# Performance work log

Measured on AMD Instinct MI355X. Metric: run time of the kernel, lower is better.

Reference implementation:

```python
import jax, jax.numpy as jnp
import numpy as np

COMMITMENT_COST = 0.25
NUM_EMBEDDINGS = 8192
EMBEDDING_DIM = 256


def setup_inputs() -> dict:
    key = jax.random.key(0)
    kx, ke = jax.random.split(key)
    x = jax.random.normal(kx, (16, 1024, EMBEDDING_DIM), dtype=jnp.float32)
    # nn.Embedding weight initialized uniform(-1/K, 1/K)
    embedding = jax.random.uniform(
        ke, (NUM_EMBEDDINGS, EMBEDDING_DIM), dtype=jnp.float32,
        minval=-1.0 / NUM_EMBEDDINGS, maxval=1.0 / NUM_EMBEDDINGS)
    return {"x": x, "embedding": embedding}


def reference(x, embedding):
    x_shape = x.shape
    D = embedding.shape[1]
    K = embedding.shape[0]
    flat_x = x.reshape(-1, D)                      # [N, D]
    N = flat_x.shape[0]

    distances = (jnp.sum(flat_x ** 2, axis=1, keepdims=True)
                 + jnp.sum(embedding ** 2, axis=1)
                 - 2.0 * jnp.matmul(flat_x, embedding.T))
    encoding_indices = jnp.argmin(distances, axis=1)  # [N]

    # one-hot @ embedding == gather
    quantized = embedding[encoding_indices].reshape(x_shape)

    sg = jax.lax.stop_gradient
    e_latent_loss = jnp.mean((sg(quantized) - x) ** 2)
    q_latent_loss = jnp.mean((quantized - sg(x)) ** 2)
    loss = q_latent_loss + COMMITMENT_COST * e_latent_loss

    # straight-through estimator
    quantized_st = x + sg(quantized - x)

    # perplexity from mean one-hot usage
    counts = jnp.zeros((K,), dtype=jnp.float32).at[encoding_indices].add(1.0)
    avg_probs = counts / N
    perplexity = jnp.exp(-jnp.sum(avg_probs * jnp.log(avg_probs + 1e-10)))

    return quantized_st.reshape(x_shape), loss, perplexity
```

## Files before the change

### kernel.cpp

```cpp
#include <hip/hip_runtime.h>


#define VQ_N 16384
#define VQ_D 256
#define VQ_K 8192

typedef __attribute__((ext_vector_type(4))) int i32x4;

#define SX 22.0f
#define SEF 1040384.0f
#define ENSCALE 11444224.0

__device__ inline int q8(float f, float scale) {
  return __float2int_rn(fminf(fmaxf(f * scale, -127.f), 127.f));
}

__global__ __launch_bounds__(256) void vq_pack(
    const float* __restrict__ E, signed char* __restrict__ Ebs,
    int* __restrict__ en_int, double* __restrict__ loss_sum,
    int* __restrict__ hist, unsigned int* __restrict__ ticket) {
  const int gid = blockIdx.x * 256 + threadIdx.x;
  if (gid < VQ_K) hist[gid] = 0;
  if (gid == 0) { *loss_sum = 0.0; *ticket = 0u; }
  const int code = gid >> 4;
  const int chunk = gid & 15;
  const float* src = E + (size_t)code * VQ_D + chunk * 16;
  double s = 0.0;
  unsigned int w[4];
#pragma unroll
  for (int v = 0; v < 4; ++v) {
    const float4 f = *(const float4*)(src + v * 4);
    s += (double)f.x * f.x + (double)f.y * f.y + (double)f.z * f.z +
         (double)f.w * f.w;
    const int q0 = q8(f.x, SEF), q1 = q8(f.y, SEF);
    const int q2 = q8(f.z, SEF), q3 = q8(f.w, SEF);
    w[v] = (unsigned)(q0 & 255) | ((unsigned)(q1 & 255) << 8) |
           ((unsigned)(q2 & 255) << 16) | ((unsigned)(q3 & 255) << 24);
  }
  const size_t off =
      ((size_t)(code >> 4) * 16 + chunk) * 256 + (size_t)(code & 15) * 16;
  *(uint4*)(Ebs + off) = make_uint4(w[0], w[1], w[2], w[3]);
#pragma unroll
  for (int m = 1; m <= 8; m <<= 1) s += __shfl_xor(s, m, 64);
  if (chunk == 0) en_int[code] = (int)__double2int_rn(s * ENSCALE);
}

__global__ __launch_bounds__(256, 1) void vq_main(
    const float* __restrict__ X, const signed char* __restrict__ Ebs,
    const int* __restrict__ en_int, const float* __restrict__ Ef,
    float* __restrict__ outq, double* __restrict__ loss_sum,
    int* __restrict__ hist, unsigned int* __restrict__ ticket,
    float* __restrict__ out) {
  __shared__ int red_s[4][64];
  __shared__ int red_i[4][64];
  __shared__ int kfin[64];
  __shared__ double wsum[4];
  __shared__ double part[256];
  __shared__ int sdone;

  const int tid = threadIdx.x;
  const int wave = tid >> 6;
  const int lane = tid & 63;
  const int quad = lane >> 4;
  const int c15 = lane & 15;
  const int r0 = blockIdx.x * 64;

  i32x4 af[4][4];
#pragma unroll
  for (int t = 0; t < 4; ++t) {
    const float* xr = X + (size_t)(r0 + t * 16 + c15) * VQ_D + quad * 16;
#pragma unroll
    for (int m = 0; m < 4; ++m) {
      const float* p = xr + m * 64;
      i32x4 pk;
#pragma unroll
      for (int v = 0; v < 4; ++v) {
        const float4 f = *(const float4*)(p + v * 4);
        const int q0 = q8(f.x, SX), q1 = q8(f.y, SX);
        const int q2 = q8(f.z, SX), q3 = q8(f.w, SX);
        pk[v] = (q0 & 255) | ((q1 & 255) << 8) | ((q2 & 255) << 16) |
                ((q3 & 255) << 24);
      }
      af[t][m] = pk;
    }
  }

  int best_s[4][4];
  int best_i[4][4];
#pragma unroll
  for (int t = 0; t < 4; ++t)
#pragma unroll
    for (int r = 0; r < 4; ++r) { best_s[t][r] = 0x7fffffff; best_i[t][r] = 0; }

  const signed char* bp =
      Ebs + (size_t)wave * 4096 + (size_t)quad * 256 + (size_t)c15 * 16;
  const int* enp = en_int + wave * 16 + c15;
  int lidx = 0;
  int ccode = wave * 16 + c15;

#define LOADB(buf, en)                                                       \
  {                                                                          \
    const signed char* p_ = bp + (size_t)lidx * 16384;                       \
    _Pragma("unroll") for (int m = 0; m < 4; ++m)                            \
        buf[m] = *(const i32x4*)(p_ + m * 1024);                             \
    en = enp[lidx * 64];                                                     \
    ++lidx;                                                                  \
  }

#define COMPUTE(buf, en)                                                     \
  {                                                                          \
    i32x4 a0 = {0, 0, 0, 0}, a1 = {0, 0, 0, 0};                              \
    i32x4 a2 = {0, 0, 0, 0}, a3 = {0, 0, 0, 0};                              \
    _Pragma("unroll") for (int m = 0; m < 4; ++m) {                          \
      a0 = __builtin_amdgcn_mfma_i32_16x16x64_i8(af[0][m], buf[m], a0, 0, 0, 0); \
      a1 = __builtin_amdgcn_mfma_i32_16x16x64_i8(af[1][m], buf[m], a1, 0, 0, 0); \
      a2 = __builtin_amdgcn_mfma_i32_16x16x64_i8(af[2][m], buf[m], a2, 0, 0, 0); \
      a3 = __builtin_amdgcn_mfma_i32_16x16x64_i8(af[3][m], buf[m], a3, 0, 0, 0); \
    }                                                                        \
    _Pragma("unroll") for (int r = 0; r < 4; ++r) {                          \
      int s;                                                                 \
      s = en - a0[r];                                                        \
      if (s < best_s[0][r]) { best_s[0][r] = s; best_i[0][r] = ccode; }      \
      s = en - a1[r];                                                        \
      if (s < best_s[1][r]) { best_s[1][r] = s; best_i[1][r] = ccode; }      \
      s = en - a2[r];                                                        \
      if (s < best_s[2][r]) { best_s[2][r] = s; best_i[2][r] = ccode; }      \
      s = en - a3[r];                                                        \
      if (s < best_s[3][r]) { best_s[3][r] = s; best_i[3][r] = ccode; }      \
    }                                                                        \
    ccode += 64;                                                             \
  }

  i32x4 bb0[4], bb1[4], bb2[4], bb3[4];
  int en0, en1, en2, en3;
  LOADB(bb0, en0); LOADB(bb1, en1); LOADB(bb2, en2); LOADB(bb3, en3);
#pragma unroll 1
  for (int i = 0; i < 124; i += 4) {
    COMPUTE(bb0, en0); LOADB(bb0, en0);
    COMPUTE(bb1, en1); LOADB(bb1, en1);
    COMPUTE(bb2, en2); LOADB(bb2, en2);
    COMPUTE(bb3, en3); LOADB(bb3, en3);
  }
  COMPUTE(bb0, en0); COMPUTE(bb1, en1); COMPUTE(bb2, en2); COMPUTE(bb3, en3);
#undef LOADB
#undef COMPUTE

#pragma unroll
  for (int t = 0; t < 4; ++t)
#pragma unroll
    for (int r = 0; r < 4; ++r) {
      int s = best_s[t][r];
      int i = best_i[t][r];
#pragma unroll
      for (int m = 1; m <= 8; m <<= 1) {
        const int os = __shfl_xor(s, m, 64);
        const int oi = __shfl_xor(i, m, 64);
        if (os < s || (os == s && oi < i)) { s = os; i = oi; }
      }
      if (c15 == 0) {
        red_s[wave][t * 16 + quad * 4 + r] = s;
        red_i[wave][t * 16 + quad * 4 + r] = i;
      }
    }
  __syncthreads();

  if (tid < 64) {
    int bs = red_s[0][tid];
    int bi = red_i[0][tid];
#pragma unroll
    for (int w = 1; w < 4; ++w) {
      const int s = red_s[w][tid];
      const int i = red_i[w][tid];
      if (s < bs || (s == bs && i < bi)) { bs = s; bi = i; }
    }
    kfin[tid] = bi;
    __hip_atomic_fetch_add(&hist[bi], 1, __ATOMIC_RELAXED,
                           __HIP_MEMORY_SCOPE_AGENT);
  }
  __syncthreads();

  double lacc = 0.0;
#pragma unroll
  for (int j = 0; j < 16; ++j) {
    const int rl = wave * 16 + j;
    const int k = kfin[rl];
    const float4 q = *(const float4*)(Ef + (size_t)k * VQ_D + lane * 4);
    const float4 x =
        *(const float4*)(X + (size_t)(r0 + rl) * VQ_D + lane * 4);
    *(float4*)(outq + (size_t)(r0 + rl) * VQ_D + lane * 4) = q;
    const double dx = (double)q.x - x.x, dy = (double)q.y - x.y;
    const double dz = (double)q.z - x.z, dw = (double)q.w - x.w;
    lacc += dx * dx + dy * dy + dz * dz + dw * dw;
  }
#pragma unroll
  for (int off = 32; off > 0; off >>= 1) lacc += __shfl_down(lacc, off, 64);
  if (lane == 0) wsum[wave] = lacc;
  __syncthreads();
  if (tid == 0) {
    atomicAdd(loss_sum, wsum[0] + wsum[1] + wsum[2] + wsum[3]);
    __threadfence();
    const unsigned int old = __hip_atomic_fetch_add(
        ticket, 1u, __ATOMIC_ACQ_REL, __HIP_MEMORY_SCOPE_AGENT);
    sdone = (old == 255u) ? 1 : 0;
  }
  __syncthreads();

  if (sdone) {
    double s = 0.0;
    for (int k = tid; k < VQ_K; k += 256) {
      const int c = __hip_atomic_load(&hist[k], __ATOMIC_RELAXED,
                                      __HIP_MEMORY_SCOPE_AGENT);
      if (c > 0) {
        const double pr = (double)c * (1.0 / (double)VQ_N);
        s += pr * log(pr + 1e-10);
      }
    }
    part[tid] = s;
    __syncthreads();
    for (int off = 128; off > 0; off >>= 1) {
      if (tid < off) part[tid] += part[tid + off];
      __syncthreads();
    }
    if (tid == 0) {
      const double ls = __hip_atomic_load(loss_sum, __ATOMIC_RELAXED,
                                          __HIP_MEMORY_SCOPE_AGENT);
      out[(size_t)VQ_N * VQ_D] =
          (float)(1.25 * ls / ((double)VQ_N * (double)VQ_D));
      out[(size_t)VQ_N * VQ_D + 1] = (float)exp(-part[0]);
    }
  }
}

extern "C" void kernel_launch(void* const* d_in, const int* in_sizes, int n_in,
                              void* d_out, int out_size, void* d_ws,
                              size_t ws_size, hipStream_t stream) {
  const float* X = (const float*)d_in[0];
  const float* E = (const float*)d_in[1];
  float* out = (float*)d_out;

  char* ws = (char*)d_ws;
  signed char* Ebs = (signed char*)ws;
  int* en_int = (int*)(ws + 2097152);
  double* loss_sum = (double*)(ws + 2129920);
  int* hist = (int*)(ws + 2129984);
  unsigned int* ticket = (unsigned int*)(ws + 2162752);

  vq_pack<<<512, 256, 0, stream>>>(E, Ebs, en_int, loss_sum, hist, ticket);
  vq_main<<<256, 256, 0, stream>>>(X, Ebs, en_int, E, out, loss_sum, hist,
                                   ticket, out);
}
```

Measured before the change: 159.7 us.

## Split codebook across blocks with LDS double-buffered staging and separate gather/finalize kernel

```diff
diff --git a/kernel.cpp b/kernel.cpp
--- a/kernel.cpp
+++ b/kernel.cpp
@@ -13,6 +13,17 @@
 
 __device__ inline int q8(float f, float scale) {
   return __float2int_rn(fminf(fmaxf(f * scale, -127.f), 127.f));
+}
+
+__device__ inline void gl_lds16(const void* g, void* l) {
+  __builtin_amdgcn_global_load_lds(
+      (const __attribute__((address_space(1))) unsigned int*)g,
+      (__attribute__((address_space(3))) unsigned int*)l, 16, 0, 0);
+}
+__device__ inline void gl_lds4(const void* g, void* l) {
+  __builtin_amdgcn_global_load_lds(
+      (const __attribute__((address_space(1))) unsigned int*)g,
+      (__attribute__((address_space(3))) unsigned int*)l, 4, 0, 0);
 }
 
 __global__ __launch_bounds__(256) void vq_pack(
@@ -45,30 +56,39 @@
   if (chunk == 0) en_int[code] = (int)__double2int_rn(s * ENSCALE);
 }
 
-__global__ __launch_bounds__(256, 1) void vq_main(
+__global__ __launch_bounds__(256, 2) void vq_score(
     const float* __restrict__ X, const signed char* __restrict__ Ebs,
-    const int* __restrict__ en_int, const float* __restrict__ Ef,
-    float* __restrict__ outq, double* __restrict__ loss_sum,
-    int* __restrict__ hist, unsigned int* __restrict__ ticket,
-    float* __restrict__ out) {
-  __shared__ int red_s[4][64];
-  __shared__ int red_i[4][64];
-  __shared__ int kfin[64];
-  __shared__ double wsum[4];
-  __shared__ double part[256];
-  __shared__ int sdone;
+    const int* __restrict__ en_int, unsigned long long* __restrict__ best64) {
+  __shared__ __align__(16) signed char bbuf[2][16384];
+  __shared__ __align__(16) int enl[1024];
 
   const int tid = threadIdx.x;
   const int wave = tid >> 6;
   const int lane = tid & 63;
   const int quad = lane >> 4;
   const int c15 = lane & 15;
-  const int r0 = blockIdx.x * 64;
+  const int rowblk = blockIdx.x >> 3;
+  const int q = blockIdx.x & 7;
+  const int r0 = rowblk * 256;
+  const int qcode = q * 1024;
+  const signed char* ebase = Ebs + (size_t)qcode * 256;
+
+  {
+    const int* ens = en_int + qcode + wave * 64 + lane;
+#pragma unroll
+    for (int j = 0; j < 4; ++j)
+      gl_lds4(ens + j * 256, enl + j * 256 + wave * 64);
+    const signed char* bs = ebase + wave * 1024 + lane * 16;
+#pragma unroll
+    for (int j = 0; j < 4; ++j)
+      gl_lds16(bs + j * 4096, &bbuf[0][j * 4096 + wave * 1024]);
+  }
 
   i32x4 af[4][4];
 #pragma unroll
   for (int t = 0; t < 4; ++t) {
-    const float* xr = X + (size_t)(r0 + t * 16 + c15) * VQ_D + quad * 16;
+    const float* xr =
+        X + (size_t)(r0 + wave * 64 + t * 16 + c15) * VQ_D + quad * 16;
 #pragma unroll
     for (int m = 0; m < 4; ++m) {
       const float* p = xr + m * 64;
@@ -76,10 +96,8 @@
 #pragma unroll
       for (int v = 0; v < 4; ++v) {
         const float4 f = *(const float4*)(p + v * 4);
-        const int q0 = q8(f.x, SX), q1 = q8(f.y, SX);
-        const int q2 = q8(f.z, SX), q3 = q8(f.w, SX);
-        pk[v] = (q0 & 255) | ((q1 & 255) << 8) | ((q2 & 255) << 16) |
-                ((q3 & 255) << 24);
+        pk[v] = (q8(f.x, SX) & 255) | ((q8(f.y, SX) & 255) << 8) |
+                ((q8(f.z, SX) & 255) << 16) | ((q8(f.w, SX) & 255) << 24);
       }
       af[t][m] = pk;
     }
@@ -92,58 +110,48 @@
 #pragma unroll
     for (int r = 0; r < 4; ++r) { best_s[t][r] = 0x7fffffff; best_i[t][r] = 0; }
 
-  const signed char* bp =
-      Ebs + (size_t)wave * 4096 + (size_t)quad * 256 + (size_t)c15 * 16;
-  const int* enp = en_int + wave * 16 + c15;
-  int lidx = 0;
-  int ccode = wave * 16 + c15;
-
-#define LOADB(buf, en)                                                       \
-  {                                                                          \
-    const signed char* p_ = bp + (size_t)lidx * 16384;                       \
-    _Pragma("unroll") for (int m = 0; m < 4; ++m)                            \
-        buf[m] = *(const i32x4*)(p_ + m * 1024);                             \
-    en = enp[lidx * 64];                                                     \
-    ++lidx;                                                                  \
-  }
-
-#define COMPUTE(buf, en)                                                     \
-  {                                                                          \
-    i32x4 a0 = {0, 0, 0, 0}, a1 = {0, 0, 0, 0};                              \
-    i32x4 a2 = {0, 0, 0, 0}, a3 = {0, 0, 0, 0};                              \
-    _Pragma("unroll") for (int m = 0; m < 4; ++m) {                          \
-      a0 = __builtin_amdgcn_mfma_i32_16x16x64_i8(af[0][m], buf[m], a0, 0, 0, 0); \
-      a1 = __builtin_amdgcn_mfma_i32_16x16x64_i8(af[1][m], buf[m], a1, 0, 0, 0); \
-      a2 = __builtin_amdgcn_mfma_i32_16x16x64_i8(af[2][m], buf[m], a2, 0, 0, 0); \
-      a3 = __builtin_amdgcn_mfma_i32_16x16x64_i8(af[3][m], buf[m], a3, 0, 0, 0); \
-    }                                                                        \
-    _Pragma("unroll") for (int r = 0; r < 4; ++r) {                          \
-      int s;                                                                 \
-      s = en - a0[r];                                                        \
-      if (s < best_s[0][r]) { best_s[0][r] = s; best_i[0][r] = ccode; }      \
-      s = en - a1[r];                                                        \
-      if (s < best_s[1][r]) { best_s[1][r] = s; best_i[1][r] = ccode; }      \
-      s = en - a2[r];                                                        \
-      if (s < best_s[2][r]) { best_s[2][r] = s; best_i[2][r] = ccode; }      \
-      s = en - a3[r];                                                        \
-      if (s < best_s[3][r]) { best_s[3][r] = s; best_i[3][r] = ccode; }      \
-    }                                                                        \
-    ccode += 64;                                                             \
-  }
-
-  i32x4 bb0[4], bb1[4], bb2[4], bb3[4];
-  int en0, en1, en2, en3;
-  LOADB(bb0, en0); LOADB(bb1, en1); LOADB(bb2, en2); LOADB(bb3, en3);
 #pragma unroll 1
-  for (int i = 0; i < 124; i += 4) {
-    COMPUTE(bb0, en0); LOADB(bb0, en0);
-    COMPUTE(bb1, en1); LOADB(bb1, en1);
-    COMPUTE(bb2, en2); LOADB(bb2, en2);
-    COMPUTE(bb3, en3); LOADB(bb3, en3);
-  }
-  COMPUTE(bb0, en0); COMPUTE(bb1, en1); COMPUTE(bb2, en2); COMPUTE(bb3, en3);
-#undef LOADB
-#undef COMPUTE
+  for (int c = 0; c < 16; ++c) {
+    __syncthreads();
+    if (c + 1 < 16) {
+      const signed char* bs =
+          ebase + (c + 1) * 16384 + wave * 1024 + lane * 16;
+#pragma unroll
+      for (int j = 0; j < 4; ++j)
+        gl_lds16(bs + j * 4096, &bbuf[(c + 1) & 1][j * 4096 + wave * 1024]);
+    }
+    const signed char* cb = &bbuf[c & 1][0];
+#pragma unroll
+    for (int g = 0; g < 4; ++g) {
+      i32x4 bfr[4];
+#pragma unroll
+      for (int m = 0; m < 4; ++m)
+        bfr[m] = *(const i32x4*)(cb + g * 4096 + m * 1024 + lane * 16);
+      const int en = enl[(c * 4 + g) * 16 + c15];
+      i32x4 a0 = {0, 0, 0, 0}, a1 = {0, 0, 0, 0};
+      i32x4 a2 = {0, 0, 0, 0}, a3 = {0, 0, 0, 0};
+#pragma unroll
+      for (int m = 0; m < 4; ++m) {
+        a0 = __builtin_amdgcn_mfma_i32_16x16x64_i8(af[0][m], bfr[m], a0, 0, 0, 0);
+        a1 = __builtin_amdgcn_mfma_i32_16x16x64_i8(af[1][m], bfr[m], a1, 0, 0, 0);
+        a2 = __builtin_amdgcn_mfma_i32_16x16x64_i8(af[2][m], bfr[m], a2, 0, 0, 0);
+        a3 = __builtin_amdgcn_mfma_i32_16x16x64_i8(af[3][m], bfr[m], a3, 0, 0, 0);
+      }
+      const int code = qcode + (c * 4 + g) * 16 + c15;
+#pragma unroll
+      for (int r = 0; r < 4; ++r) {
+        int s;
+        s = en - a0[r];
+        if (s < best_s[0][r]) { best_s[0][r] = s; best_i[0][r] = code; }
+        s = en - a1[r];
+        if (s < best_s[1][r]) { best_s[1][r] = s; best_i[1][r] = code; }
+        s = en - a2[r];
+        if (s < best_s[2][r]) { best_s[2][r] = s; best_i[2][r] = code; }
+        s = en - a3[r];
+        if (s < best_s[3][r]) { best_s[3][r] = s; best_i[3][r] = code; }
+      }
+    }
+  }
 
 #pragma unroll
   for (int t = 0; t < 4; ++t)
@@ -158,56 +166,64 @@
         if (os < s || (os == s && oi < i)) { s = os; i = oi; }
       }
       if (c15 == 0) {
-        red_s[wave][t * 16 + quad * 4 + r] = s;
-        red_i[wave][t * 16 + quad * 4 + r] = i;
-      }
-    }
+        const int row = r0 + wave * 64 + t * 16 + quad * 4 + r;
+        best64[(size_t)q * VQ_N + row] =
+            ((unsigned long long)((unsigned)s ^ 0x80000000u) << 32) |
+            (unsigned)i;
+      }
+    }
+}
+
+__global__ __launch_bounds__(256) void vq_gather_fin(
+    const float* __restrict__ X, const float* __restrict__ E,
+    const unsigned long long* __restrict__ best64, float* __restrict__ outq,
+    double* __restrict__ loss_sum, int* __restrict__ hist,
+    unsigned int* __restrict__ ticket, float* __restrict__ out) {
+  __shared__ double wsum[4];
+  __shared__ double part[256];
+  __shared__ int sdone;
+  const int wid = threadIdx.x >> 6;
+  const int lane = threadIdx.x & 63;
+  const int gw = blockIdx.x * 4 + wid;
+  double acc = 0.0;
+#pragma unroll 4
+  for (int row = gw; row < VQ_N; row += 2048) {
+    unsigned long long v =
+        (lane < 8) ? best64[(size_t)lane * VQ_N + row] : ~0ULL;
+#pragma unroll
+    for (int m = 1; m <= 4; m <<= 1) {
+      const unsigned long long ov = __shfl_xor(v, m, 64);
+      if (ov < v) v = ov;
+    }
+    v = __shfl(v, 0, 64);
+    const int k = (int)(v & 0xFFFFFFFFu);
+    if (lane == 0)
+      __hip_atomic_fetch_add(&hist[k], 1, __ATOMIC_RELAXED,
+                             __HIP_MEMORY_SCOPE_AGENT);
+    const float4 qv = *(const float4*)(E + (size_t)k * VQ_D + lane * 4);
+    const float4 xv = *(const float4*)(X + (size_t)row * VQ_D + lane * 4);
+    *(float4*)(outq + (size_t)row * VQ_D + lane * 4) = qv;
+    const double dx = (double)qv.x - xv.x, dy = (double)qv.y - xv.y;
+    const double dz = (double)qv.z - xv.z, dw = (double)qv.w - xv.w;
+    acc += dx * dx + dy * dy + dz * dz + dw * dw;
+  }
+#pragma unroll
+  for (int off = 32; off > 0; off >>= 1) acc += __shfl_down(acc, off, 64);
+  if (lane == 0) wsum[wid] = acc;
   __syncthreads();
-
-  if (tid < 64) {
-    int bs = red_s[0][tid];
-    int bi = red_i[0][tid];
-#pragma unroll
-    for (int w = 1; w < 4; ++w) {
-      const int s = red_s[w][tid];
-      const int i = red_i[w][tid];
-      if (s < bs || (s == bs && i < bi)) { bs = s; bi = i; }
-    }
-    kfin[tid] = bi;
-    __hip_atomic_fetch_add(&hist[bi], 1, __ATOMIC_RELAXED,
-                           __HIP_MEMORY_SCOPE_AGENT);
-  }
-  __syncthreads();
-
-  double lacc = 0.0;
-#pragma unroll
-  for (int j = 0; j < 16; ++j) {
-    const int rl = wave * 16 + j;
-    const int k = kfin[rl];
-    const float4 q = *(const float4*)(Ef + (size_t)k * VQ_D + lane * 4);
-    const float4 x =
-        *(const float4*)(X + (size_t)(r0 + rl) * VQ_D + lane * 4);
-    *(float4*)(outq + (size_t)(r0 + rl) * VQ_D + lane * 4) = q;
-    const double dx = (double)q.x - x.x, dy = (double)q.y - x.y;
-    const double dz = (double)q.z - x.z, dw = (double)q.w - x.w;
-    lacc += dx * dx + dy * dy + dz * dz + dw * dw;
-  }
-#pragma unroll
-  for (int off = 32; off > 0; off >>= 1) lacc += __shfl_down(lacc, off, 64);
-  if (lane == 0) wsum[wave] = lacc;
-  __syncthreads();
-  if (tid == 0) {
+  if (threadIdx.x == 0) {
     atomicAdd(loss_sum, wsum[0] + wsum[1] + wsum[2] + wsum[3]);
     __threadfence();
     const unsigned int old = __hip_atomic_fetch_add(
         ticket, 1u, __ATOMIC_ACQ_REL, __HIP_MEMORY_SCOPE_AGENT);
-    sdone = (old == 255u) ? 1 : 0;
+    sdone = (old == 511u) ? 1 : 0;
   }
   __syncthreads();
 
   if (sdone) {
+    const int tx = threadIdx.x;
     double s = 0.0;
-    for (int k = tid; k < VQ_K; k += 256) {
+    for (int k = tx; k < VQ_K; k += 256) {
       const int c = __hip_atomic_load(&hist[k], __ATOMIC_RELAXED,
                                       __HIP_MEMORY_SCOPE_AGENT);
       if (c > 0) {
@@ -215,13 +231,13 @@
         s += pr * log(pr + 1e-10);
       }
     }
-    part[tid] = s;
+    part[tx] = s;
     __syncthreads();
     for (int off = 128; off > 0; off >>= 1) {
-      if (tid < off) part[tid] += part[tid + off];
+      if (tx < off) part[tx] += part[tx + off];
       __syncthreads();
     }
-    if (tid == 0) {
+    if (tx == 0) {
       const double ls = __hip_atomic_load(loss_sum, __ATOMIC_RELAXED,
                                           __HIP_MEMORY_SCOPE_AGENT);
       out[(size_t)VQ_N * VQ_D] =
@@ -244,8 +260,11 @@
   double* loss_sum = (double*)(ws + 2129920);
   int* hist = (int*)(ws + 2129984);
   unsigned int* ticket = (unsigned int*)(ws + 2162752);
+  unsigned long long* best64 =
+      (unsigned long long*)(ws + 2162816);
 
   vq_pack<<<512, 256, 0, stream>>>(E, Ebs, en_int, loss_sum, hist, ticket);
-  vq_main<<<256, 256, 0, stream>>>(X, Ebs, en_int, E, out, loss_sum, hist,
-                                   ticket, out);
-}
+  vq_score<<<512, 256, 0, stream>>>(X, Ebs, en_int, best64);
+  vq_gather_fin<<<512, 256, 0, stream>>>(X, E, best64, out, loss_sum, hist,
+                                         ticket, out);
+}
```

After: 178.1 us. 11.5% more time.
